# Optimization experiments

Measured on AMD Instinct MI355X. Metric: run time of the kernel, lower is better.

Reference implementation:

```python
import jax, jax.numpy as jnp
import numpy as np

EPS = 1e-5
KERNELS = [3, 3, 5, 7]  # 2*i+1 for i>=1, first layer k=3


def _conv_relu_bn(x, w, b, gamma, beta, rmean, rvar):
    # x: [B, Cin, S], w: [Cout, Cin, K]
    k = w.shape[-1]
    y = jax.lax.conv_general_dilated(
        x, w, window_strides=(1,), padding=[(k // 2, k // 2)],
        dimension_numbers=("NCW", "OIW", "NCW"))
    y = y + b[None, :, None]
    y = jax.nn.relu(y)
    # BatchNorm1d in inference mode (running stats)
    inv = gamma[None, :, None] / jnp.sqrt(rvar[None, :, None] + EPS)
    return (y - rmean[None, :, None]) * inv + beta[None, :, None]


def setup_inputs() -> dict:
    key = jax.random.key(0)
    ks = jax.random.split(key, 32)
    B, S = 128, 8192
    inp = {"x": jax.random.normal(ks[0], (B, 4, S), dtype=jnp.float32)}
    cin = 4
    for i, k in enumerate(KERNELS):
        inp[f"w{i}"] = jax.random.normal(ks[1 + i], (32, cin, k), dtype=jnp.float32) * 0.1
        inp[f"b{i}"] = jnp.zeros((32,), jnp.float32)
        inp[f"g{i}"] = jnp.ones((32,), jnp.float32)   # BN gamma
        inp[f"bb{i}"] = jnp.zeros((32,), jnp.float32)  # BN beta
        inp[f"rm{i}"] = jnp.zeros((32,), jnp.float32)  # running mean
        inp[f"rv{i}"] = jnp.ones((32,), jnp.float32)   # running var
        cin = 32
    inp["fw1"] = jax.random.normal(ks[10], (16, 32), dtype=jnp.float32) * 0.1
    inp["fb1"] = jnp.zeros((16,), jnp.float32)
    inp["fw2"] = jax.random.normal(ks[11], (1, 16), dtype=jnp.float32) * 0.1
    inp["fb2"] = jnp.zeros((1,), jnp.float32)
    return inp


def reference(x,
              w0, b0, g0, bb0, rm0, rv0,
              w1, b1, g1, bb1, rm1, rv1,
              w2, b2, g2, bb2, rm2, rv2,
              w3, b3, g3, bb3, rm3, rv3,
              fw1, fb1, fw2, fb2):
    x = _conv_relu_bn(x, w0, b0, g0, bb0, rm0, rv0)
    x = _conv_relu_bn(x, w1, b1, g1, bb1, rm1, rv1)
    x = _conv_relu_bn(x, w2, b2, g2, bb2, rm2, rv2)
    x = _conv_relu_bn(x, w3, b3, g3, bb3, rm3, rv3)
    # [B, 32, S] -> [B, S, 32]; the original per-timestep MLP loop is one batched GEMM
    h = jnp.einsum("bcs,hc->bsh", x, fw1) + fb1
    h = jax.nn.relu(h)  # Dropout(0.1) is identity in eval
    out = jnp.einsum("bsh,oh->bso", h, fw2) + fb2
    return out[..., 0]  # squeeze(-1) -> [B, S]
```

## Files before the change

### kernel.cpp

```cpp
#include <hip/hip_runtime.h>

#define SEQ    8192
#define S_TILE 244
#define NROW   264
#define CS     2120
#define NTHR   512
#define NREC   37
#define BN_HALFOFF (NREC*512)

typedef __attribute__((ext_vector_type(8))) _Float16 half8;
typedef __attribute__((ext_vector_type(4))) _Float16 half4v;
typedef __attribute__((ext_vector_type(4))) float    f32x4;

__device__ __forceinline__ int uni(int v){ return __builtin_amdgcn_readfirstlane(v); }

extern "C" __global__ void prep_kernel(
    const float* w0, const float* w1, const float* w2, const float* w3,
    const float* b0, const float* g0, const float* bb0, const float* rm0, const float* rv0,
    const float* b1, const float* g1, const float* bb1, const float* rm1, const float* rv1,
    const float* b2, const float* g2, const float* bb2, const float* rm2, const float* rv2,
    const float* b3, const float* g3, const float* bb3, const float* rm3, const float* rv3,
    const float* fw1, _Float16* ws)
{
    const int tid  = threadIdx.x;
    const int lane = tid & 63;
    for (int rec = tid >> 6; rec < NREC; rec += 4) {
        const float* W; int CIN, K, r2;
        if      (rec < 6)  { W = w0;  CIN = 4;  K = 3; r2 = rec;      }
        else if (rec < 12) { W = w1;  CIN = 32; K = 3; r2 = rec - 6;  }
        else if (rec < 22) { W = w2;  CIN = 32; K = 5; r2 = rec - 12; }
        else if (rec < 36) { W = w3;  CIN = 32; K = 7; r2 = rec - 22; }
        else               { W = fw1; CIN = 32; K = 1; r2 = 0;        }
        int tap = r2 >> 1, mh = r2 & 1;
        int co  = mh*16 + (lane & 15);
        int ci0 = (lane >> 4) * 8;
        half8 h;
#pragma unroll
        for (int j = 0; j < 8; ++j) {
            int ci = ci0 + j;
            float wv = (ci < CIN) ? W[(co*CIN + ci)*K + tap] : 0.0f;
            h[j] = (_Float16)wv;
        }
        *(half8*)(ws + rec*512 + lane*8) = h;
    }
    if (tid < 128) {
        int l = tid >> 5, co = tid & 31;
        const float *g, *bb, *rm, *rv, *bi;
        if      (l == 0) { g=g0; bb=bb0; rm=rm0; rv=rv0; bi=b0; }
        else if (l == 1) { g=g1; bb=bb1; rm=rm1; rv=rv1; bi=b1; }
        else if (l == 2) { g=g2; bb=bb2; rm=rm2; rv=rv2; bi=b2; }
        else             { g=g3; bb=bb3; rm=rm3; rv=rv3; bi=b3; }
        float scale = g[co] / sqrtf(rv[co] + 1e-5f);
        float shift = bb[co] - rm[co]*scale;
        float* bn = (float*)(ws + BN_HALFOFF) + (l*32 + co)*4;
        bn[0] = scale; bn[1] = shift; bn[2] = bi[co]; bn[3] = 0.0f;
    }
}

template<int K, int DOFF>
__device__ __forceinline__ void conv_layer(
    const _Float16* __restrict__ rec, const float4* __restrict__ bn,
    const _Float16* in, _Float16* outb, int s0, int ntb, int lane)
{
    const int q = lane >> 4, n = lane & 15;
    f32x4 acc[2][2];
#pragma unroll
    for (int nt = 0; nt < 2; ++nt)
#pragma unroll
        for (int mh = 0; mh < 2; ++mh) acc[nt][mh] = (f32x4){0.f, 0.f, 0.f, 0.f};

#pragma unroll
    for (int tap = 0; tap < K; ++tap) {
        half8 a0 = *(const half8*)(rec + (tap*2 + 0)*512 + lane*8);
        half8 a1 = *(const half8*)(rec + (tap*2 + 1)*512 + lane*8);
#pragma unroll
        for (int nt = 0; nt < 2; ++nt) {
            int pos = (ntb + nt)*16 + n + tap;
            half8 bf = *(const half8*)(in + q*CS + pos*8);
            acc[nt][0] = __builtin_amdgcn_mfma_f32_16x16x32_f16(a0, bf, acc[nt][0], 0, 0, 0);
            acc[nt][1] = __builtin_amdgcn_mfma_f32_16x16x32_f16(a1, bf, acc[nt][1], 0, 0, 0);
        }
    }
#pragma unroll
    for (int nt = 0; nt < 2; ++nt) {
        int pos = (ntb + nt)*16 + n;
        bool oob = (unsigned)(s0 + DOFF + pos) >= SEQ;
#pragma unroll
        for (int mh = 0; mh < 2; ++mh) {
            int co0 = mh*16 + q*4;
            half4v hv;
#pragma unroll
            for (int r = 0; r < 4; ++r) {
                float4 p = bn[co0 + r];
                float v = fmaxf(acc[nt][mh][r] + p.z, 0.0f)*p.x + p.y;
                if (oob) v = 0.0f;
                hv[r] = (_Float16)v;
            }
            int cb = mh*2 + (q >> 1);
            *(half4v*)(outb + cb*CS + pos*8 + (q & 1)*4) = hv;
        }
    }
}

extern "C" __global__ void __launch_bounds__(NTHR, 6)
dnashape_mfma(const float* __restrict__ x, const _Float16* __restrict__ ws,
              const float* __restrict__ fb1, const float* __restrict__ fw2,
              const float* __restrict__ fb2, float* __restrict__ out)
{
    __shared__ _Float16 bufA[4*CS];
    __shared__ _Float16 bufB[4*CS];

    const int tid  = threadIdx.x;
    const int tile = blockIdx.x, b = blockIdx.y;
    const int s0   = tile * S_TILE;

    const half8 z8 = {0,0,0,0,0,0,0,0};
    for (int li = tid; li < NROW; li += NTHR) {
        int sg = s0 - 7 + li;
        bool ok = (unsigned)sg < SEQ;
        float v0 = ok ? x[(b*4 + 0)*SEQ + sg] : 0.f;
        float v1 = ok ? x[(b*4 + 1)*SEQ + sg] : 0.f;
        float v2 = ok ? x[(b*4 + 2)*SEQ + sg] : 0.f;
        float v3 = ok ? x[(b*4 + 3)*SEQ + sg] : 0.f;
        half8 h0 = {(_Float16)v0, (_Float16)v1, (_Float16)v2, (_Float16)v3, 0, 0, 0, 0};
        *(half8*)(bufB + 0*CS + li*8) = h0;
        *(half8*)(bufB + 1*CS + li*8) = z8;
        *(half8*)(bufB + 2*CS + li*8) = z8;
        *(half8*)(bufB + 3*CS + li*8) = z8;
    }
    if (tid < 32) *(half8*)(bufA + (tid >> 3)*CS + (256 + (tid & 7))*8) = z8;
    __syncthreads();

    const int lane = tid & 63;
    const int ntb  = uni(tid >> 6) * 2;
    const float4* bn = (const float4*)(ws + BN_HALFOFF);

    conv_layer<3, -6>(ws +  0*512, bn +  0, bufB, bufA, s0, ntb, lane);
    __syncthreads();
    conv_layer<3, -5>(ws +  6*512, bn + 32, bufA, bufB, s0, ntb, lane);
    __syncthreads();
    conv_layer<5, -3>(ws + 12*512, bn + 64, bufB, bufA, s0, ntb, lane);
    __syncthreads();
    conv_layer<7,  0>(ws + 22*512, bn + 96, bufA, bufB, s0, ntb, lane);
    __syncthreads();

    {
        const int q = lane >> 4, n = lane & 15;
        half8 am = *(const half8*)(ws + 36*512 + lane*8);
        float fb1v[4], fw2v[4];
#pragma unroll
        for (int r = 0; r < 4; ++r) { fb1v[r] = fb1[q*4 + r]; fw2v[r] = fw2[q*4 + r]; }
        float fb2v = fb2[0];
#pragma unroll
        for (int nt = 0; nt < 2; ++nt) {
            int pos = (ntb + nt)*16 + n;
            half8 bf = *(const half8*)(bufB + q*CS + pos*8);
            f32x4 d = {0.f, 0.f, 0.f, 0.f};
            d = __builtin_amdgcn_mfma_f32_16x16x32_f16(am, bf, d, 0, 0, 0);
            float part = 0.f;
#pragma unroll
            for (int r = 0; r < 4; ++r) part += fmaxf(d[r] + fb1v[r], 0.f)*fw2v[r];
            part += __shfl_xor(part, 16, 64);
            part += __shfl_xor(part, 32, 64);
            if (lane < 16) {
                int g = s0 + pos;
                if (pos < S_TILE && g < SEQ) out[b*SEQ + g] = part + fb2v;
            }
        }
    }
}

extern "C" void kernel_launch(void* const* d_in, const int* in_sizes, int n_in,
                              void* d_out, int out_size, void* d_ws, size_t ws_size,
                              hipStream_t stream) {
    const float* p[29];
    for (int i = 0; i < 29; ++i) p[i] = (const float*)d_in[i];
    _Float16* ws = (_Float16*)d_ws;

    prep_kernel<<<1, 256, 0, stream>>>(
        p[1], p[7], p[13], p[19],
        p[2], p[3], p[4], p[5], p[6],
        p[8], p[9], p[10], p[11], p[12],
        p[14], p[15], p[16], p[17], p[18],
        p[20], p[21], p[22], p[23], p[24],
        p[25], ws);

    dim3 grid((SEQ + S_TILE - 1) / S_TILE, 128);
    dnashape_mfma<<<grid, NTHR, 0, stream>>>(p[0], (const _Float16*)ws,
                                             p[26], p[27], p[28], (float*)d_out);
}
```

Baseline: 205.8 us.

## Fuse weight prep into main kernel, staging packed weights in LDS per layer

```diff
diff --git a/kernel.cpp b/kernel.cpp
--- a/kernel.cpp
+++ b/kernel.cpp
@@ -5,8 +5,6 @@
 #define NROW   264
 #define CS     2120
 #define NTHR   512
-#define NREC   37
-#define BN_HALFOFF (NREC*512)
 
 typedef __attribute__((ext_vector_type(8))) _Float16 half8;
 typedef __attribute__((ext_vector_type(4))) _Float16 half4v;
@@ -14,23 +12,12 @@
 
 __device__ __forceinline__ int uni(int v){ return __builtin_amdgcn_readfirstlane(v); }
 
-extern "C" __global__ void prep_kernel(
-    const float* w0, const float* w1, const float* w2, const float* w3,
-    const float* b0, const float* g0, const float* bb0, const float* rm0, const float* rv0,
-    const float* b1, const float* g1, const float* bb1, const float* rm1, const float* rv1,
-    const float* b2, const float* g2, const float* bb2, const float* rm2, const float* rv2,
-    const float* b3, const float* g3, const float* bb3, const float* rm3, const float* rv3,
-    const float* fw1, _Float16* ws)
+__device__ __forceinline__ void build_recs(const float* __restrict__ W,
+                                           int CIN, int K, int nrec,
+                                           _Float16* dst, int tid)
 {
-    const int tid  = threadIdx.x;
-    const int lane = tid & 63;
-    for (int rec = tid >> 6; rec < NREC; rec += 4) {
-        const float* W; int CIN, K, r2;
-        if      (rec < 6)  { W = w0;  CIN = 4;  K = 3; r2 = rec;      }
-        else if (rec < 12) { W = w1;  CIN = 32; K = 3; r2 = rec - 6;  }
-        else if (rec < 22) { W = w2;  CIN = 32; K = 5; r2 = rec - 12; }
-        else if (rec < 36) { W = w3;  CIN = 32; K = 7; r2 = rec - 22; }
-        else               { W = fw1; CIN = 32; K = 1; r2 = 0;        }
+    for (int idx = tid; idx < nrec * 64; idx += NTHR) {
+        int r2 = idx >> 6, lane = idx & 63;
         int tap = r2 >> 1, mh = r2 & 1;
         int co  = mh*16 + (lane & 15);
         int ci0 = (lane >> 4) * 8;
@@ -38,31 +25,20 @@
 #pragma unroll
         for (int j = 0; j < 8; ++j) {
             int ci = ci0 + j;
-            float wv = (ci < CIN) ? W[(co*CIN + ci)*K + tap] : 0.0f;
-            h[j] = (_Float16)wv;
+            h[j] = (_Float16)((ci < CIN) ? W[(co*CIN + ci)*K + tap] : 0.0f);
         }
-        *(half8*)(ws + rec*512 + lane*8) = h;
-    }
-    if (tid < 128) {
-        int l = tid >> 5, co = tid & 31;
-        const float *g, *bb, *rm, *rv, *bi;
-        if      (l == 0) { g=g0; bb=bb0; rm=rm0; rv=rv0; bi=b0; }
-        else if (l == 1) { g=g1; bb=bb1; rm=rm1; rv=rv1; bi=b1; }
-        else if (l == 2) { g=g2; bb=bb2; rm=rm2; rv=rv2; bi=b2; }
-        else             { g=g3; bb=bb3; rm=rm3; rv=rv3; bi=b3; }
-        float scale = g[co] / sqrtf(rv[co] + 1e-5f);
-        float shift = bb[co] - rm[co]*scale;
-        float* bn = (float*)(ws + BN_HALFOFF) + (l*32 + co)*4;
-        bn[0] = scale; bn[1] = shift; bn[2] = bi[co]; bn[3] = 0.0f;
+        *(half8*)(dst + r2*512 + lane*8) = h;
     }
 }
 
 template<int K, int DOFF>
 __device__ __forceinline__ void conv_layer(
-    const _Float16* __restrict__ rec, const float4* __restrict__ bn,
+    const _Float16* rec, const float4* bn,
     const _Float16* in, _Float16* outb, int s0, int ntb, int lane)
 {
     const int q = lane >> 4, n = lane & 15;
+    const _Float16* bbase = in + q*CS + (ntb*16 + n)*8;
+
     f32x4 acc[2][2];
 #pragma unroll
     for (int nt = 0; nt < 2; ++nt)
@@ -75,12 +51,12 @@
         half8 a1 = *(const half8*)(rec + (tap*2 + 1)*512 + lane*8);
 #pragma unroll
         for (int nt = 0; nt < 2; ++nt) {
-            int pos = (ntb + nt)*16 + n + tap;
-            half8 bf = *(const half8*)(in + q*CS + pos*8);
+            half8 bf = *(const half8*)(bbase + nt*128 + tap*8);
             acc[nt][0] = __builtin_amdgcn_mfma_f32_16x16x32_f16(a0, bf, acc[nt][0], 0, 0, 0);
             acc[nt][1] = __builtin_amdgcn_mfma_f32_16x16x32_f16(a1, bf, acc[nt][1], 0, 0, 0);
         }
     }
+
 #pragma unroll
     for (int nt = 0; nt < 2; ++nt) {
         int pos = (ntb + nt)*16 + n;
@@ -102,11 +78,23 @@
     }
 }
 
-extern "C" __global__ void __launch_bounds__(NTHR, 6)
-dnashape_mfma(const float* __restrict__ x, const _Float16* __restrict__ ws,
-              const float* __restrict__ fb1, const float* __restrict__ fw2,
-              const float* __restrict__ fb2, float* __restrict__ out)
+extern "C" __global__ void __launch_bounds__(NTHR, 4)
+dnashape_mfma(const float* __restrict__ x,
+    const float* __restrict__ w0, const float* __restrict__ b0, const float* __restrict__ g0,
+    const float* __restrict__ bb0, const float* __restrict__ rm0, const float* __restrict__ rv0,
+    const float* __restrict__ w1, const float* __restrict__ b1, const float* __restrict__ g1,
+    const float* __restrict__ bb1, const float* __restrict__ rm1, const float* __restrict__ rv1,
+    const float* __restrict__ w2, const float* __restrict__ b2, const float* __restrict__ g2,
+    const float* __restrict__ bb2, const float* __restrict__ rm2, const float* __restrict__ rv2,
+    const float* __restrict__ w3, const float* __restrict__ b3, const float* __restrict__ g3,
+    const float* __restrict__ bb3, const float* __restrict__ rm3, const float* __restrict__ rv3,
+    const float* __restrict__ fw1, const float* __restrict__ fb1,
+    const float* __restrict__ fw2, const float* __restrict__ fb2,
+    float* __restrict__ out)
 {
+    __shared__ _Float16 recA[10*512];
+    __shared__ _Float16 recB[14*512];
+    __shared__ float4   bnL[128];
     __shared__ _Float16 bufA[4*CS];
     __shared__ _Float16 bufB[4*CS];
 
@@ -129,24 +117,41 @@
         *(half8*)(bufB + 3*CS + li*8) = z8;
     }
     if (tid < 32) *(half8*)(bufA + (tid >> 3)*CS + (256 + (tid & 7))*8) = z8;
+
+    build_recs(w0, 4,  3, 6, recA, tid);
+    build_recs(w1, 32, 3, 6, recB, tid);
+    if (tid < 128) {
+        int l = tid >> 5, co = tid & 31;
+        const float *g, *bb, *rm, *rv, *bi;
+        if      (l == 0) { g=g0; bb=bb0; rm=rm0; rv=rv0; bi=b0; }
+        else if (l == 1) { g=g1; bb=bb1; rm=rm1; rv=rv1; bi=b1; }
+        else if (l == 2) { g=g2; bb=bb2; rm=rm2; rv=rv2; bi=b2; }
+        else             { g=g3; bb=bb3; rm=rm3; rv=rv3; bi=b3; }
+        float scale = g[co] / sqrtf(rv[co] + 1e-5f);
+        float shift = bb[co] - rm[co]*scale;
+        float4 v; v.x = scale; v.y = shift; v.z = bi[co]; v.w = 0.f;
+        bnL[l*32 + co] = v;
+    }
     __syncthreads();
 
     const int lane = tid & 63;
     const int ntb  = uni(tid >> 6) * 2;
-    const float4* bn = (const float4*)(ws + BN_HALFOFF);
 
-    conv_layer<3, -6>(ws +  0*512, bn +  0, bufB, bufA, s0, ntb, lane);
+    conv_layer<3, -6>(recA, bnL +  0, bufB, bufA, s0, ntb, lane);
     __syncthreads();
-    conv_layer<3, -5>(ws +  6*512, bn + 32, bufA, bufB, s0, ntb, lane);
+    conv_layer<3, -5>(recB, bnL + 32, bufA, bufB, s0, ntb, lane);
+    build_recs(w2, 32, 5, 10, recA, tid);
     __syncthreads();
-    conv_layer<5, -3>(ws + 12*512, bn + 64, bufB, bufA, s0, ntb, lane);
+    conv_layer<5, -3>(recA, bnL + 64, bufB, bufA, s0, ntb, lane);
+    build_recs(w3, 32, 7, 14, recB, tid);
     __syncthreads();
-    conv_layer<7,  0>(ws + 22*512, bn + 96, bufA, bufB, s0, ntb, lane);
+    conv_layer<7,  0>(recB, bnL + 96, bufA, bufB, s0, ntb, lane);
+    build_recs(fw1, 32, 1, 1, recA, tid);
     __syncthreads();
 
     {
         const int q = lane >> 4, n = lane & 15;
-        half8 am = *(const half8*)(ws + 36*512 + lane*8);
+        half8 am = *(const half8*)(recA + lane*8);
         float fb1v[4], fw2v[4];
 #pragma unroll
         for (int r = 0; r < 4; ++r) { fb1v[r] = fb1[q*4 + r]; fw2v[r] = fw2[q*4 + r]; }
@@ -175,17 +180,12 @@
                               hipStream_t stream) {
     const float* p[29];
     for (int i = 0; i < 29; ++i) p[i] = (const float*)d_in[i];
-    _Float16* ws = (_Float16*)d_ws;
-
-    prep_kernel<<<1, 256, 0, stream>>>(
-        p[1], p[7], p[13], p[19],
-        p[2], p[3], p[4], p[5], p[6],
-        p[8], p[9], p[10], p[11], p[12],
-        p[14], p[15], p[16], p[17], p[18],
-        p[20], p[21], p[22], p[23], p[24],
-        p[25], ws);
-
     dim3 grid((SEQ + S_TILE - 1) / S_TILE, 128);
-    dnashape_mfma<<<grid, NTHR, 0, stream>>>(p[0], (const _Float16*)ws,
-                                             p[26], p[27], p[28], (float*)d_out);
+    dnashape_mfma<<<grid, NTHR, 0, stream>>>(p[0],
+        p[1],  p[2],  p[3],  p[4],  p[5],  p[6],
+        p[7],  p[8],  p[9],  p[10], p[11], p[12],
+        p[13], p[14], p[15], p[16], p[17], p[18],
+        p[19], p[20], p[21], p[22], p[23], p[24],
+        p[25], p[26], p[27], p[28],
+        (float*)d_out);
 }
```

Result: slower. 274.6 us (+33.4%).
